# Performance work log

Hardware: AMD Instinct MI355X
Metric: run time of the kernel (lower is better)

## Reference

```python
import jax, jax.numpy as jnp
import numpy as np

NUM_PROTEINS = 19000
NUM_DRUGS = 4000
NUM_CELL_LINES = 16
BATCH = 4096
NUM_EDGES = 40000
LAYERS = [2048, 1024, 1]
IN_DIM = 2 * (NUM_PROTEINS + NUM_CELL_LINES)  # 38032


def setup_inputs() -> dict:
    key = jax.random.key(0)
    ks = jax.random.split(key, 10)
    inp = {
        "drug_pairs": jax.random.randint(ks[0], (BATCH, 2), 0, NUM_DRUGS, dtype=jnp.int64 if jax.config.jax_enable_x64 else jnp.int32),
        "cell_lines": jax.random.randint(ks[1], (BATCH,), 0, NUM_CELL_LINES),
        "dpi_drug": jax.random.randint(ks[2], (NUM_EDGES,), 0, NUM_DRUGS),
        "dpi_prot": jax.random.randint(ks[3], (NUM_EDGES,), 0, NUM_PROTEINS),
        "W0": jax.random.normal(ks[4], (LAYERS[0], IN_DIM), dtype=jnp.float32) * 0.02,
        "b0": jnp.zeros((LAYERS[0],), dtype=jnp.float32),
        "W1": jax.random.normal(ks[5], (LAYERS[1], LAYERS[0]), dtype=jnp.float32) * 0.02,
        "b1": jnp.zeros((LAYERS[1],), dtype=jnp.float32),
        "W2": jax.random.normal(ks[6], (LAYERS[2], LAYERS[1]), dtype=jnp.float32) * 0.02,
        "b2": jnp.zeros((LAYERS[2],), dtype=jnp.float32),
    }
    return inp


def _mlp(x, W0, b0, W1, b1, W2, b2):
    h = jax.nn.relu(x @ W0.T + b0)
    h = jax.nn.relu(h @ W1.T + b1)
    return h @ W2.T + b2


def reference(drug_pairs, cell_lines, dpi_drug, dpi_prot, W0, b0, W1, b1, W2, b2):
    # Build drug -> protein multi-hot table with a single vectorized scatter
    # (replaces the per-row Python loop: prot[i, targets] = 1)
    table = jnp.zeros((NUM_DRUGS, NUM_PROTEINS), dtype=jnp.float32)
    table = table.at[dpi_drug, dpi_prot].set(1.0)

    prot_1 = table[drug_pairs[:, 0]]  # [B, P]
    prot_2 = table[drug_pairs[:, 1]]  # [B, P]
    one_hot_cl = jax.nn.one_hot(cell_lines, NUM_CELL_LINES, dtype=jnp.float32)  # [B, C]

    bd1 = jnp.concatenate([prot_1, one_hot_cl], axis=1)
    bd2 = jnp.concatenate([prot_2, one_hot_cl], axis=1)
    x1 = jnp.concatenate([bd1, bd2], axis=1)  # [B, 2*(P+C)]
    x2 = jnp.concatenate([bd2, bd1], axis=1)

    out1 = _mlp(x1, W0, b0, W1, b1, W2, b2)
    out2 = _mlp(x2, W0, b0, W1, b1, W2, b2)
    return (out1[:, 0], out2[:, 0])
```

## Files before the change

kernel.cpp:

```cpp
#include <hip/hip_runtime.h>
#include <hip/hip_bf16.h>
#include <stdint.h>

#define NPROT 19000
#define NDRUG 4000
#define NCELL 16
#define BATCH 4096
#define NEDGE 40000
#define L0 2048
#define L1DIM 1024
#define INDIM 38032
#define HALFDIM 19016
#define WSTN 19008
#define DCAP 96
#define BMWORDS ((NDRUG * NPROT + 31) / 32)

typedef float f32x4 __attribute__((ext_vector_type(4)));
typedef short s16x8 __attribute__((ext_vector_type(8)));

__global__ void zero_all_kernel(int* __restrict__ p, int n) {
    int i = blockIdx.x * 256 + threadIdx.x;
    if (i < n) p[i] = 0;
}

__global__ void scatter_dedup_kernel(const int* __restrict__ drug, const int* __restrict__ prot,
                                     unsigned* __restrict__ bitmap, int* __restrict__ cnt,
                                     unsigned short* __restrict__ dlist) {
    int e = blockIdx.x * 256 + threadIdx.x;
    if (e < NEDGE) {
        int d = drug[e], p = prot[e];
        unsigned idx = (unsigned)d * NPROT + p;
        unsigned bit = 1u << (idx & 31u);
        unsigned old = atomicOr(&bitmap[idx >> 5], bit);
        if (!(old & bit)) {
            int pos = atomicAdd(&cnt[d], 1);
            if (pos < DCAP) dlist[d * DCAP + pos] = (unsigned short)p;
        }
    }
}

__global__ __launch_bounds__(512) void stream_meta_kernel(const int* __restrict__ cnt,
                                                          int* __restrict__ wlen,
                                                          int* __restrict__ wbase,
                                                          int* __restrict__ pref,
                                                          int* __restrict__ tcnt) {
    __shared__ int wl[8];
    int t = threadIdx.x;
    if (t < 8) wl[t] = 0;
    __syncthreads();
    int c = 0;
#pragma unroll
    for (int k = 0; k < 8; ++k) {
        int d = t + (k << 9);
        pref[t * 8 + k] = c;
        if (d < NDRUG) c += max(min(cnt[d], DCAP), 1);
    }
    tcnt[t] = c;
    atomicMax(&wl[t >> 6], c);
    __syncthreads();
    if (t == 0) {
        int run = 0;
        for (int w = 0; w < 8; ++w) {
            wlen[w] = wl[w];
            wbase[w] = run;
            run += wl[w] * 64;
        }
    }
}

__global__ __launch_bounds__(256) void fill_stream_kernel(const int* __restrict__ cnt,
                                                          const unsigned short* __restrict__ dlist,
                                                          const int* __restrict__ wbase,
                                                          const int* __restrict__ wlen,
                                                          const int* __restrict__ pref,
                                                          const int* __restrict__ tcnt,
                                                          unsigned short* __restrict__ estream) {
    int g = blockIdx.x * 256 + threadIdx.x;
    if (g < NDRUG) {
        int d = g;
        int t = d & 511, k = d >> 9;
        int base = wbase[t >> 6] + (t & 63);
        int idx = pref[t * 8 + k];
        int n = min(cnt[d], DCAP);
        if (n == 0) {
            estream[base + idx * 64] = (unsigned short)(19000 | 0x8000);
        } else {
            for (int i = 0; i < n; ++i) {
                unsigned short e = dlist[d * DCAP + i];
                if (i == n - 1) e |= 0x8000;
                estream[base + (idx + i) * 64] = e;
            }
        }
    } else if (g < NDRUG + 512) {
        int t = g - NDRUG;
        int base = wbase[t >> 6] + (t & 63);
        int wl = wlen[t >> 6];
        for (int idx = tcnt[t]; idx < wl; ++idx)
            estream[base + idx * 64] = (unsigned short)19000;
    }
}

__global__ void base_kernel(const float* __restrict__ W0, const float* __restrict__ b0,
                            float* __restrict__ BASE) {
    int i = blockIdx.x * 256 + threadIdx.x;
    if (i < NCELL * L0) {
        int c = i >> 11, ch = i & 2047;
        const float* wr = W0 + (size_t)ch * INDIM;
        BASE[(size_t)c * L0 + ch] = b0[ch] + wr[NPROT + c] + wr[HALFDIM + NPROT + c];
    }
}

__device__ inline unsigned bfpair(float a, float b) {
    unsigned ua = __float_as_uint(a), ub = __float_as_uint(b);
    ua += 0x7fffu + ((ua >> 16) & 1u);
    ub += 0x7fffu + ((ub >> 16) & 1u);
    return (ua >> 16) | (ub & 0xffff0000u);
}
__device__ inline float bflo(unsigned w) { return __uint_as_float(w << 16); }
__device__ inline float bfhi(unsigned w) { return __uint_as_float(w & 0xffff0000u); }

__global__ __launch_bounds__(512) void drug_sum_kernel(const float* __restrict__ W0,
                                                       const unsigned short* __restrict__ estream,
                                                       const int* __restrict__ wbase,
                                                       const int* __restrict__ wlen,
                                                       __hip_bfloat16* __restrict__ SAb,
                                                       __hip_bfloat16* __restrict__ SBb) {
    __shared__ uint2 wst[WSTN];
    int t = threadIdx.x;
    int bid = blockIdx.x;
    int j = bid & 7;
    int k2 = bid >> 3;
    int ch4 = k2 & 3;
    int ghi = k2 >> 2;
    int group = j + 8 * ghi;
    int hb = group >> 7;
    int line = group & 127;
    int ch0 = line * 16 + ch4 * 4;
    size_t colbase = (size_t)hb * HALFDIM;

    int wv = t >> 6;
    int base = wbase[wv] + (t & 63);
    int wl = wlen[wv];
    int nfull = wl >> 3, rem = wl & 7;
    unsigned e[8];
    if (nfull > 0) {
#pragma unroll
        for (int k = 0; k < 8; ++k) e[k] = estream[base + k * 64];
        base += 512;
    }

    const float* sA = W0 + (size_t)(ch0 + 0) * INDIM + colbase;
    const float* sB = W0 + (size_t)(ch0 + 1) * INDIM + colbase;
    const float* sC = W0 + (size_t)(ch0 + 2) * INDIM + colbase;
    const float* sD = W0 + (size_t)(ch0 + 3) * INDIM + colbase;
    for (int i = t * 4; i < 19000; i += 2048) {
        float4 a = *(const float4*)(sA + i);
        float4 b = *(const float4*)(sB + i);
        float4 c = *(const float4*)(sC + i);
        float4 d = *(const float4*)(sD + i);
        uint4 q0, q1;
        q0.x = bfpair(a.x, b.x); q0.y = bfpair(c.x, d.x);
        q0.z = bfpair(a.y, b.y); q0.w = bfpair(c.y, d.y);
        q1.x = bfpair(a.z, b.z); q1.y = bfpair(c.z, d.z);
        q1.z = bfpair(a.w, b.w); q1.w = bfpair(c.w, d.w);
        *(uint4*)&wst[i] = q0;
        *(uint4*)&wst[i + 2] = q1;
    }
    if (t < 8) { wst[19000 + t].x = 0u; wst[19000 + t].y = 0u; }
    __syncthreads();

    float x0 = 0.f, x1 = 0.f, x2 = 0.f, x3 = 0.f;
    int kk = 0;
    __hip_bfloat16* dst = (hb ? SBb : SAb) + ch0;

    auto process = [&](const unsigned* ev) {
#pragma unroll
        for (int k = 0; k < 8; ++k) {
            uint2 w = wst[ev[k] & 0x7fffu];
            x0 += bflo(w.x);
            x1 += bfhi(w.x);
            x2 += bflo(w.y);
            x3 += bfhi(w.y);
            if (ev[k] & 0x8000u) {
                uint2 v;
                v.x = bfpair(x0, x1);
                v.y = bfpair(x2, x3);
                *(uint2*)&dst[(size_t)(t + (kk << 9)) * L0] = v;
                ++kk; x0 = 0.f; x1 = 0.f; x2 = 0.f; x3 = 0.f;
            }
        }
    };

    if (nfull > 0) {
        for (int it = 1; it < nfull; ++it) {
            unsigned f[8];
#pragma unroll
            for (int k = 0; k < 8; ++k) f[k] = estream[base + k * 64];
            base += 512;
            process(e);
#pragma unroll
            for (int k = 0; k < 8; ++k) e[k] = f[k];
        }
        process(e);
    }
    for (int k = 0; k < rem; ++k) {
        unsigned ev = estream[base + k * 64];
        uint2 w = wst[ev & 0x7fffu];
        x0 += bflo(w.x);
        x1 += bfhi(w.x);
        x2 += bflo(w.y);
        x3 += bfhi(w.y);
        if (ev & 0x8000u) {
            uint2 v;
            v.x = bfpair(x0, x1);
            v.y = bfpair(x2, x3);
            *(uint2*)&dst[(size_t)(t + (kk << 9)) * L0] = v;
            ++kk; x0 = 0.f; x1 = 0.f; x2 = 0.f; x3 = 0.f;
        }
    }
}

__global__ void cvtw1_kernel(const float* __restrict__ W1, __hip_bfloat16* __restrict__ W1b) {
    int i = blockIdx.x * 256 + threadIdx.x;
    const int n = L1DIM * L0 / 4;
    if (i < n) {
        float4 v = ((const float4*)W1)[i];
        uint2 q;
        q.x = bfpair(v.x, v.y);
        q.y = bfpair(v.z, v.w);
        ((uint2*)W1b)[i] = q;
    }
}

__global__ __launch_bounds__(256) void build_h_kernel(const int* __restrict__ dp,
                                                      const int* __restrict__ cl,
                                                      const __hip_bfloat16* __restrict__ SAb,
                                                      const __hip_bfloat16* __restrict__ SBb,
                                                      const float* __restrict__ BASE,
                                                      __hip_bfloat16* __restrict__ h1) {
    int b = blockIdx.x;
    int d1 = dp[2 * b], d2 = dp[2 * b + 1], c = cl[b];
    int ch = threadIdx.x * 8;
    const float* bs = BASE + (size_t)c * L0 + ch;
    uint4 ua1 = *(const uint4*)(SAb + (size_t)d1 * L0 + ch);
    uint4 ua2 = *(const uint4*)(SAb + (size_t)d2 * L0 + ch);
    uint4 us1 = *(const uint4*)(SBb + (size_t)d1 * L0 + ch);
    uint4 us2 = *(const uint4*)(SBb + (size_t)d2 * L0 + ch);
    float4 vb0 = *(const float4*)(bs);
    float4 vb1 = *(const float4*)(bs + 4);
    float bsv[8] = {vb0.x, vb0.y, vb0.z, vb0.w, vb1.x, vb1.y, vb1.z, vb1.w};
    unsigned a1w[4] = {ua1.x, ua1.y, ua1.z, ua1.w};
    unsigned a2w[4] = {ua2.x, ua2.y, ua2.z, ua2.w};
    unsigned s1w[4] = {us1.x, us1.y, us1.z, us1.w};
    unsigned s2w[4] = {us2.x, us2.y, us2.z, us2.w};
    float z1[8], z2[8];
#pragma unroll
    for (int k = 0; k < 4; ++k) {
        z1[2 * k]     = fmaxf(bsv[2 * k]     + bflo(a1w[k]) + bflo(s2w[k]), 0.f);
        z1[2 * k + 1] = fmaxf(bsv[2 * k + 1] + bfhi(a1w[k]) + bfhi(s2w[k]), 0.f);
        z2[2 * k]     = fmaxf(bsv[2 * k]     + bflo(a2w[k]) + bflo(s1w[k]), 0.f);
        z2[2 * k + 1] = fmaxf(bsv[2 * k + 1] + bfhi(a2w[k]) + bfhi(s1w[k]), 0.f);
    }
    uint4 o1, o2;
    o1.x = bfpair(z1[0], z1[1]); o1.y = bfpair(z1[2], z1[3]);
    o1.z = bfpair(z1[4], z1[5]); o1.w = bfpair(z1[6], z1[7]);
    o2.x = bfpair(z2[0], z2[1]); o2.y = bfpair(z2[2], z2[3]);
    o2.z = bfpair(z2[4], z2[5]); o2.w = bfpair(z2[6], z2[7]);
    *(uint4*)((__hip_bfloat16*)h1 + (size_t)b * L0 + ch) = o1;
    *(uint4*)((__hip_bfloat16*)h1 + (size_t)(BATCH + b) * L0 + ch) = o2;
}

__global__ void init_out_kernel(float* __restrict__ out, const float* __restrict__ b2, int n) {
    int i = blockIdx.x * 256 + threadIdx.x;
    if (i < n) out[i] = b2[0];
}

#define BM 128
#define BN 128
#define BK2 64
__global__ __launch_bounds__(256) void gemm_kernel(const __hip_bfloat16* __restrict__ A,
                                                   const __hip_bfloat16* __restrict__ B,
                                                   const float* __restrict__ bias,
                                                   const float* __restrict__ W2,
                                                   float* __restrict__ out,
                                                   int M, int N, int K) {
    __shared__ __hip_bfloat16 As[BM * BK2];
    __shared__ __hip_bfloat16 Bs[BN * BK2];
    int t = threadIdx.x;
    int bid = blockIdx.x;
    int xcd = bid & 7, ii2 = bid >> 3;
    int by = xcd * 8 + (ii2 >> 3);
    int bx = ii2 & 7;
    int brow = by * BM, bcol = bx * BN;
    int w = t >> 6, l = t & 63;
    int wr = w >> 1, wc = w & 1;
    f32x4 acc[4][4] = {};
    int row = l & 15, ko = (l >> 4) * 8;
    int swz = (row & 7) * 8;
    for (int k0 = 0; k0 < K; k0 += BK2) {
#pragma unroll
        for (int i = 0; i < 4; ++i) {
            int idx = i * 256 + t;
            int r = idx >> 3;
            int cb = ((idx & 7) ^ (r & 7)) * 8;
            __builtin_amdgcn_global_load_lds(
                (const __attribute__((address_space(1))) void*)(A + (size_t)(brow + r) * K + k0 + cb),
                (__attribute__((address_space(3))) void*)(&As[idx * 8]), 16, 0, 0);
            __builtin_amdgcn_global_load_lds(
                (const __attribute__((address_space(1))) void*)(B + (size_t)(bcol + r) * K + k0 + cb),
                (__attribute__((address_space(3))) void*)(&Bs[idx * 8]), 16, 0, 0);
        }
        __syncthreads();
#pragma unroll
        for (int ks = 0; ks < 2; ++ks) {
            int col = (ks * 32 + ko) ^ swz;
            s16x8 af[4], bfr[4];
#pragma unroll
            for (int m = 0; m < 4; ++m)
                af[m] = *(const s16x8*)(&As[(wr * 64 + m * 16 + row) * BK2 + col]);
#pragma unroll
            for (int n = 0; n < 4; ++n)
                bfr[n] = *(const s16x8*)(&Bs[(wc * 64 + n * 16 + row) * BK2 + col]);
#pragma unroll
            for (int m = 0; m < 4; ++m)
#pragma unroll
                for (int n = 0; n < 4; ++n)
                    acc[m][n] = __builtin_amdgcn_mfma_f32_16x16x32_bf16(af[m], bfr[n], acc[m][n], 0, 0, 0);
        }
        __syncthreads();
    }
    int cr = (l >> 4) * 4;
    int cc = l & 15;
#pragma unroll
    for (int m = 0; m < 4; ++m) {
        float s[4] = {0.f, 0.f, 0.f, 0.f};
#pragma unroll
        for (int n = 0; n < 4; ++n) {
            int gcol = bcol + wc * 64 + n * 16 + cc;
            float bv = bias[gcol];
            float wv = W2[gcol];
#pragma unroll
            for (int j = 0; j < 4; ++j) {
                float v = fmaxf(acc[m][n][j] + bv, 0.f);
                s[j] += v * wv;
            }
        }
#pragma unroll
        for (int mask = 1; mask < 16; mask <<= 1) {
#pragma unroll
            for (int j = 0; j < 4; ++j) s[j] += __shfl_xor(s[j], mask);
        }
        if (cc == 0) {
            int grow = brow + wr * 64 + m * 16 + cr;
#pragma unroll
            for (int j = 0; j < 4; ++j) atomicAdd(&out[grow + j], s[j]);
        }
    }
}

extern "C" void kernel_launch(void* const* d_in, const int* in_sizes, int n_in,
                              void* d_out, int out_size, void* d_ws, size_t ws_size,
                              hipStream_t stream) {
    const int* drug_pairs = (const int*)d_in[0];
    const int* cell_lines = (const int*)d_in[1];
    const int* dpi_drug = (const int*)d_in[2];
    const int* dpi_prot = (const int*)d_in[3];
    const float* W0 = (const float*)d_in[4];
    const float* b0 = (const float*)d_in[5];
    const float* W1 = (const float*)d_in[6];
    const float* b1 = (const float*)d_in[7];
    const float* W2 = (const float*)d_in[8];
    const float* b2 = (const float*)d_in[9];
    float* out = (float*)d_out;

    char* ws = (char*)d_ws;
    size_t off = 0;
    auto alloc = [&](size_t bytes) {
        char* p = ws + off;
        off += (bytes + 255) & ~(size_t)255;
        return p;
    };
    __hip_bfloat16* SAb = (__hip_bfloat16*)alloc((size_t)NDRUG * L0 * 2);
    __hip_bfloat16* SBb = (__hip_bfloat16*)alloc((size_t)NDRUG * L0 * 2);
    float* BASE = (float*)alloc((size_t)NCELL * L0 * 4);
    __hip_bfloat16* W1b = (__hip_bfloat16*)alloc((size_t)L1DIM * L0 * 2);
    __hip_bfloat16* h1 = (__hip_bfloat16*)alloc((size_t)2 * BATCH * L0 * 2);
    const int ZREG_N = BMWORDS + NDRUG;
    int* zreg = (int*)alloc((size_t)ZREG_N * 4);
    unsigned* bitmap = (unsigned*)zreg;
    int* cnt = zreg + BMWORDS;
    unsigned short* dlist = (unsigned short*)alloc((size_t)NDRUG * DCAP * 2);
    int* wlen = (int*)alloc(8 * 4);
    int* wbase = (int*)alloc(8 * 4);
    int* pref = (int*)alloc((size_t)512 * 8 * 4);
    int* tcnt = (int*)alloc((size_t)512 * 4);
    unsigned short* estream = (unsigned short*)alloc((size_t)64 * (NEDGE + NDRUG + 512) * 2);

    zero_all_kernel<<<(ZREG_N + 255) / 256, 256, 0, stream>>>(zreg, ZREG_N);
    scatter_dedup_kernel<<<(NEDGE + 255) / 256, 256, 0, stream>>>(dpi_drug, dpi_prot,
                                                                  bitmap, cnt, dlist);
    stream_meta_kernel<<<1, 512, 0, stream>>>(cnt, wlen, wbase, pref, tcnt);
    fill_stream_kernel<<<(NDRUG + 512 + 255) / 256, 256, 0, stream>>>(cnt, dlist, wbase,
                                                                      wlen, pref, tcnt, estream);
    base_kernel<<<(NCELL * L0 + 255) / 256, 256, 0, stream>>>(W0, b0, BASE);
    drug_sum_kernel<<<L0 / 2, 512, 0, stream>>>(W0, estream, wbase, wlen, SAb, SBb);
    cvtw1_kernel<<<(L1DIM * L0 / 4 + 255) / 256, 256, 0, stream>>>(W1, W1b);
    build_h_kernel<<<BATCH, 256, 0, stream>>>(drug_pairs, cell_lines, SAb, SBb, BASE, h1);
    init_out_kernel<<<(2 * BATCH + 255) / 256, 256, 0, stream>>>(out, b2, 2 * BATCH);
    gemm_kernel<<<(2 * BATCH / BM) * (L1DIM / BN), 256, 0, stream>>>(h1, W1b, b1, W2, out,
                                                                     2 * BATCH, L1DIM, L0);
}
```

Before: 224.5 us.

## Write drug sums channel-major then transpose to drug-major in separate kernel

The drug-sum kernel now writes per-drug 4-channel results contiguously along the drug index for each channel quad, instead of strided scatter writes with a 4096-byte stride. A new tiled shared-memory transpose kernel converts these into the drug-major layout that build_h expects. The W0 staging loop is also unrolled with a peeled tail. This removes the uncoalesced scattered stores but adds an extra kernel launch and an extra round trip through memory for the 32 MB of intermediate data.

Measured after the change: 228.9 us. About the same (+2.0%).

```diff
diff --git a/kernel.cpp b/kernel.cpp
--- a/kernel.cpp
+++ b/kernel.cpp
@@ -14,6 +14,7 @@
 #define WSTN 19008
 #define DCAP 96
 #define BMWORDS ((NDRUG * NPROT + 31) / 32)
+#define NQUAD 512
 
 typedef float f32x4 __attribute__((ext_vector_type(4)));
 typedef short s16x8 __attribute__((ext_vector_type(8)));
@@ -123,19 +124,14 @@
                                                        const unsigned short* __restrict__ estream,
                                                        const int* __restrict__ wbase,
                                                        const int* __restrict__ wlen,
-                                                       __hip_bfloat16* __restrict__ SAb,
-                                                       __hip_bfloat16* __restrict__ SBb) {
+                                                       uint2* __restrict__ SAT,
+                                                       uint2* __restrict__ SBT) {
     __shared__ uint2 wst[WSTN];
     int t = threadIdx.x;
     int bid = blockIdx.x;
-    int j = bid & 7;
-    int k2 = bid >> 3;
-    int ch4 = k2 & 3;
-    int ghi = k2 >> 2;
-    int group = j + 8 * ghi;
-    int hb = group >> 7;
-    int line = group & 127;
-    int ch0 = line * 16 + ch4 * 4;
+    int hb = bid >> 9;
+    int k2 = bid & 511;
+    int ch0 = k2 * 4;
     size_t colbase = (size_t)hb * HALFDIM;
 
     int wv = t >> 6;
@@ -153,7 +149,9 @@
     const float* sB = W0 + (size_t)(ch0 + 1) * INDIM + colbase;
     const float* sC = W0 + (size_t)(ch0 + 2) * INDIM + colbase;
     const float* sD = W0 + (size_t)(ch0 + 3) * INDIM + colbase;
-    for (int i = t * 4; i < 19000; i += 2048) {
+#pragma unroll
+    for (int k = 0; k < 9; ++k) {
+        int i = t * 4 + k * 2048;
         float4 a = *(const float4*)(sA + i);
         float4 b = *(const float4*)(sB + i);
         float4 c = *(const float4*)(sC + i);
@@ -166,12 +164,28 @@
         *(uint4*)&wst[i] = q0;
         *(uint4*)&wst[i + 2] = q1;
     }
+    {
+        int i = t * 4 + 9 * 2048;
+        if (i < 19000) {
+            float4 a = *(const float4*)(sA + i);
+            float4 b = *(const float4*)(sB + i);
+            float4 c = *(const float4*)(sC + i);
+            float4 d = *(const float4*)(sD + i);
+            uint4 q0, q1;
+            q0.x = bfpair(a.x, b.x); q0.y = bfpair(c.x, d.x);
+            q0.z = bfpair(a.y, b.y); q0.w = bfpair(c.y, d.y);
+            q1.x = bfpair(a.z, b.z); q1.y = bfpair(c.z, d.z);
+            q1.z = bfpair(a.w, b.w); q1.w = bfpair(c.w, d.w);
+            *(uint4*)&wst[i] = q0;
+            *(uint4*)&wst[i + 2] = q1;
+        }
+    }
     if (t < 8) { wst[19000 + t].x = 0u; wst[19000 + t].y = 0u; }
     __syncthreads();
 
     float x0 = 0.f, x1 = 0.f, x2 = 0.f, x3 = 0.f;
     int kk = 0;
-    __hip_bfloat16* dst = (hb ? SBb : SAb) + ch0;
+    uint2* dstT = (hb ? SBT : SAT) + (size_t)k2 * NDRUG;
 
     auto process = [&](const unsigned* ev) {
 #pragma unroll
@@ -185,7 +199,7 @@
                 uint2 v;
                 v.x = bfpair(x0, x1);
                 v.y = bfpair(x2, x3);
-                *(uint2*)&dst[(size_t)(t + (kk << 9)) * L0] = v;
+                dstT[t + (kk << 9)] = v;
                 ++kk; x0 = 0.f; x1 = 0.f; x2 = 0.f; x3 = 0.f;
             }
         }
@@ -214,10 +228,34 @@
             uint2 v;
             v.x = bfpair(x0, x1);
             v.y = bfpair(x2, x3);
-            *(uint2*)&dst[(size_t)(t + (kk << 9)) * L0] = v;
+            dstT[t + (kk << 9)] = v;
             ++kk; x0 = 0.f; x1 = 0.f; x2 = 0.f; x3 = 0.f;
         }
     }
+}
+
+__global__ __launch_bounds__(256) void transpose_kernel(const uint2* __restrict__ SAT,
+                                                        const uint2* __restrict__ SBT,
+                                                        uint2* __restrict__ SAb,
+                                                        uint2* __restrict__ SBb) {
+    __shared__ uint2 tile[32][33];
+    const int KT = NQUAD / 32;
+    const int DT = NDRUG / 32;
+    int b = blockIdx.x;
+    int half = b / (KT * DT);
+    int rem = b % (KT * DT);
+    int k0 = (rem / DT) * 32;
+    int d0 = (rem % DT) * 32;
+    const uint2* in = half ? SBT : SAT;
+    uint2* out = half ? SBb : SAb;
+    int tx = threadIdx.x & 31, ty = threadIdx.x >> 5;
+#pragma unroll
+    for (int r = 0; r < 32; r += 8)
+        tile[r + ty][tx] = in[(size_t)(k0 + r + ty) * NDRUG + d0 + tx];
+    __syncthreads();
+#pragma unroll
+    for (int r = 0; r < 32; r += 8)
+        out[(size_t)(d0 + r + ty) * NQUAD + k0 + tx] = tile[tx][r + ty];
 }
 
 __global__ void cvtw1_kernel(const float* __restrict__ W1, __hip_bfloat16* __restrict__ W1b) {
@@ -382,6 +420,8 @@
     };
     __hip_bfloat16* SAb = (__hip_bfloat16*)alloc((size_t)NDRUG * L0 * 2);
     __hip_bfloat16* SBb = (__hip_bfloat16*)alloc((size_t)NDRUG * L0 * 2);
+    uint2* SAT = (uint2*)alloc((size_t)NQUAD * NDRUG * 8);
+    uint2* SBT = (uint2*)alloc((size_t)NQUAD * NDRUG * 8);
     float* BASE = (float*)alloc((size_t)NCELL * L0 * 4);
     __hip_bfloat16* W1b = (__hip_bfloat16*)alloc((size_t)L1DIM * L0 * 2);
     __hip_bfloat16* h1 = (__hip_bfloat16*)alloc((size_t)2 * BATCH * L0 * 2);
@@ -403,7 +443,9 @@
     fill_stream_kernel<<<(NDRUG + 512 + 255) / 256, 256, 0, stream>>>(cnt, dlist, wbase,
                                                                       wlen, pref, tcnt, estream);
     base_kernel<<<(NCELL * L0 + 255) / 256, 256, 0, stream>>>(W0, b0, BASE);
-    drug_sum_kernel<<<L0 / 2, 512, 0, stream>>>(W0, estream, wbase, wlen, SAb, SBb);
+    drug_sum_kernel<<<2 * NQUAD, 512, 0, stream>>>(W0, estream, wbase, wlen, SAT, SBT);
+    transpose_kernel<<<2 * (NQUAD / 32) * (NDRUG / 32), 256, 0, stream>>>(SAT, SBT,
+                                                                          (uint2*)SAb, (uint2*)SBb);
     cvtw1_kernel<<<(L1DIM * L0 / 4 + 255) / 256, 256, 0, stream>>>(W1, W1b);
     build_h_kernel<<<BATCH, 256, 0, stream>>>(drug_pairs, cell_lines, SAb, SBb, BASE, h1);
     init_out_kernel<<<(2 * BATCH + 255) / 256, 256, 0, stream>>>(out, b2, 2 * BATCH);
```

## Per-channel fp32 drug sums via direct global-to-LDS loads plus separate transpose

Applied to the files above, without the earlier changes.

The drug_sum kernel now processes one W0 row per block (4096 blocks) instead of four channels packed as bf16 pairs. It stages the row into LDS with global_load_lds (no register round-trip or bf16 packing) and accumulates in fp32 with branchless per-event stores into a channel-major scratch buffer. A new transpose kernel converts that scratch into the drug-major bf16 SAb/SBb layout. The aim is to remove the strided scattered 8-byte stores and the conversion ALU work. In exchange it adds a roughly 75 MB fp32 scratch write and read, re-reads the edge stream four times as often, and stores on every event rather than only at segment ends.

New measurement: 314.4 us. 40.1% more time.

```diff
diff --git a/kernel.cpp b/kernel.cpp
--- a/kernel.cpp
+++ b/kernel.cpp
@@ -11,9 +11,9 @@
 #define L1DIM 1024
 #define INDIM 38032
 #define HALFDIM 19016
-#define WSTN 19008
 #define DCAP 96
 #define BMWORDS ((NDRUG * NPROT + 31) / 32)
+#define SLOTS 4608
 
 typedef float f32x4 __attribute__((ext_vector_type(4)));
 typedef short s16x8 __attribute__((ext_vector_type(8)));
@@ -123,20 +123,12 @@
                                                        const unsigned short* __restrict__ estream,
                                                        const int* __restrict__ wbase,
                                                        const int* __restrict__ wlen,
-                                                       __hip_bfloat16* __restrict__ SAb,
-                                                       __hip_bfloat16* __restrict__ SBb) {
-    __shared__ uint2 wst[WSTN];
+                                                       float* __restrict__ SAT) {
+    __shared__ float wst[19008];
     int t = threadIdx.x;
     int bid = blockIdx.x;
-    int j = bid & 7;
-    int k2 = bid >> 3;
-    int ch4 = k2 & 3;
-    int ghi = k2 >> 2;
-    int group = j + 8 * ghi;
-    int hb = group >> 7;
-    int line = group & 127;
-    int ch0 = line * 16 + ch4 * 4;
-    size_t colbase = (size_t)hb * HALFDIM;
+    int hb = bid >> 11;
+    int ch = bid & 2047;
 
     int wv = t >> 6;
     int base = wbase[wv] + (t & 63);
@@ -149,46 +141,24 @@
         base += 512;
     }
 
-    const float* sA = W0 + (size_t)(ch0 + 0) * INDIM + colbase;
-    const float* sB = W0 + (size_t)(ch0 + 1) * INDIM + colbase;
-    const float* sC = W0 + (size_t)(ch0 + 2) * INDIM + colbase;
-    const float* sD = W0 + (size_t)(ch0 + 3) * INDIM + colbase;
+    const float* src = W0 + (size_t)ch * INDIM + (size_t)hb * HALFDIM;
     for (int i = t * 4; i < 19000; i += 2048) {
-        float4 a = *(const float4*)(sA + i);
-        float4 b = *(const float4*)(sB + i);
-        float4 c = *(const float4*)(sC + i);
-        float4 d = *(const float4*)(sD + i);
-        uint4 q0, q1;
-        q0.x = bfpair(a.x, b.x); q0.y = bfpair(c.x, d.x);
-        q0.z = bfpair(a.y, b.y); q0.w = bfpair(c.y, d.y);
-        q1.x = bfpair(a.z, b.z); q1.y = bfpair(c.z, d.z);
-        q1.z = bfpair(a.w, b.w); q1.w = bfpair(c.w, d.w);
-        *(uint4*)&wst[i] = q0;
-        *(uint4*)&wst[i + 2] = q1;
-    }
-    if (t < 8) { wst[19000 + t].x = 0u; wst[19000 + t].y = 0u; }
+        __builtin_amdgcn_global_load_lds(
+            (const __attribute__((address_space(1))) void*)(src + i),
+            (__attribute__((address_space(3))) void*)(&wst[i]), 16, 0, 0);
+    }
+    if (t < 8) wst[19000 + t] = 0.f;
     __syncthreads();
 
-    float x0 = 0.f, x1 = 0.f, x2 = 0.f, x3 = 0.f;
+    float x = 0.f;
     int kk = 0;
-    __hip_bfloat16* dst = (hb ? SBb : SAb) + ch0;
-
-    auto process = [&](const unsigned* ev) {
-#pragma unroll
-        for (int k = 0; k < 8; ++k) {
-            uint2 w = wst[ev[k] & 0x7fffu];
-            x0 += bflo(w.x);
-            x1 += bfhi(w.x);
-            x2 += bflo(w.y);
-            x3 += bfhi(w.y);
-            if (ev[k] & 0x8000u) {
-                uint2 v;
-                v.x = bfpair(x0, x1);
-                v.y = bfpair(x2, x3);
-                *(uint2*)&dst[(size_t)(t + (kk << 9)) * L0] = v;
-                ++kk; x0 = 0.f; x1 = 0.f; x2 = 0.f; x3 = 0.f;
-            }
-        }
+    float* dstT = SAT + (size_t)bid * SLOTS;
+
+    auto proc = [&](unsigned ev) {
+        x += wst[ev & 0x7fffu];
+        dstT[t + (kk << 9)] = x;
+        kk += (int)(ev >> 15);
+        x = (ev & 0x8000u) ? 0.f : x;
     };
 
     if (nfull > 0) {
@@ -197,26 +167,44 @@
 #pragma unroll
             for (int k = 0; k < 8; ++k) f[k] = estream[base + k * 64];
             base += 512;
-            process(e);
+#pragma unroll
+            for (int k = 0; k < 8; ++k) proc(e[k]);
 #pragma unroll
             for (int k = 0; k < 8; ++k) e[k] = f[k];
         }
-        process(e);
+#pragma unroll
+        for (int k = 0; k < 8; ++k) proc(e[k]);
     }
     for (int k = 0; k < rem; ++k) {
         unsigned ev = estream[base + k * 64];
-        uint2 w = wst[ev & 0x7fffu];
-        x0 += bflo(w.x);
-        x1 += bfhi(w.x);
-        x2 += bflo(w.y);
-        x3 += bfhi(w.y);
-        if (ev & 0x8000u) {
-            uint2 v;
-            v.x = bfpair(x0, x1);
-            v.y = bfpair(x2, x3);
-            *(uint2*)&dst[(size_t)(t + (kk << 9)) * L0] = v;
-            ++kk; x0 = 0.f; x1 = 0.f; x2 = 0.f; x3 = 0.f;
-        }
+        proc(ev);
+    }
+}
+
+__global__ __launch_bounds__(256) void transpose_kernel(const float* __restrict__ SAT,
+                                                        __hip_bfloat16* __restrict__ SAb,
+                                                        __hip_bfloat16* __restrict__ SBb) {
+    __shared__ float tile[32][33];
+    const int CT = 2048 / 32;
+    const int DT = NDRUG / 32;
+    int b = blockIdx.x;
+    int hb = b / (CT * DT);
+    int rem = b % (CT * DT);
+    int c0 = (rem / DT) * 32;
+    int d0 = (rem % DT) * 32;
+    const float* in = SAT + (size_t)hb * 2048 * SLOTS;
+    __hip_bfloat16* out = hb ? SBb : SAb;
+    int tx = threadIdx.x & 31, ty = threadIdx.x >> 5;
+#pragma unroll
+    for (int r = 0; r < 32; r += 8)
+        tile[r + ty][tx] = in[(size_t)(c0 + r + ty) * SLOTS + d0 + tx];
+    __syncthreads();
+    int cp = threadIdx.x & 15, rw = threadIdx.x >> 4;
+#pragma unroll
+    for (int rr = 0; rr < 32; rr += 16) {
+        int r = rw + rr;
+        unsigned wq = bfpair(tile[cp * 2][r], tile[cp * 2 + 1][r]);
+        *(unsigned*)((__hip_bfloat16*)out + (size_t)(d0 + r) * L0 + c0 + cp * 2) = wq;
     }
 }
 
@@ -382,6 +370,7 @@
     };
     __hip_bfloat16* SAb = (__hip_bfloat16*)alloc((size_t)NDRUG * L0 * 2);
     __hip_bfloat16* SBb = (__hip_bfloat16*)alloc((size_t)NDRUG * L0 * 2);
+    float* SAT = (float*)alloc((size_t)4096 * SLOTS * 4);
     float* BASE = (float*)alloc((size_t)NCELL * L0 * 4);
     __hip_bfloat16* W1b = (__hip_bfloat16*)alloc((size_t)L1DIM * L0 * 2);
     __hip_bfloat16* h1 = (__hip_bfloat16*)alloc((size_t)2 * BATCH * L0 * 2);
@@ -403,7 +392,8 @@
     fill_stream_kernel<<<(NDRUG + 512 + 255) / 256, 256, 0, stream>>>(cnt, dlist, wbase,
                                                                       wlen, pref, tcnt, estream);
     base_kernel<<<(NCELL * L0 + 255) / 256, 256, 0, stream>>>(W0, b0, BASE);
-    drug_sum_kernel<<<L0 / 2, 512, 0, stream>>>(W0, estream, wbase, wlen, SAb, SBb);
+    drug_sum_kernel<<<4096, 512, 0, stream>>>(W0, estream, wbase, wlen, SAT);
+    transpose_kernel<<<2 * 64 * (NDRUG / 32), 256, 0, stream>>>(SAT, SAb, SBb);
     cvtw1_kernel<<<(L1DIM * L0 / 4 + 255) / 256, 256, 0, stream>>>(W1, W1b);
     build_h_kernel<<<BATCH, 256, 0, stream>>>(drug_pairs, cell_lines, SAb, SBb, BASE, h1);
     init_out_kernel<<<(2 * BATCH + 255) / 256, 256, 0, stream>>>(out, b2, 2 * BATCH);
```
